# Kernel optimization log

Hardware: AMD Instinct MI355X
Metric: run time of the kernel (lower is better)

The kernel has to match this reference:

```python
import jax, jax.numpy as jnp
import numpy as np

INPUT_SIZE = 512
HIDDEN_SIZE = 512
BATCH = 16384


def setup_inputs() -> dict:
    key = jax.random.key(0)
    ks = jax.random.split(key, 11)
    stdv = 1.0 / np.sqrt(HIDDEN_SIZE)
    in_dim = INPUT_SIZE + HIDDEN_SIZE

    def unif(k, shape):
        return jax.random.uniform(k, shape, jnp.float32, -stdv, stdv)

    inp = {
        "input_": jax.random.normal(ks[0], (BATCH, INPUT_SIZE), jnp.float32),
        "prev_h": jax.random.normal(ks[1], (BATCH, HIDDEN_SIZE), jnp.float32),
        "prev_c": jax.random.normal(ks[2], (BATCH, HIDDEN_SIZE), jnp.float32),
        # gate weights in torch nn.Linear layout: (out=hidden, in=input+hidden)
        "W_i": unif(ks[3], (HIDDEN_SIZE, in_dim)),
        "b_i": unif(ks[4], (HIDDEN_SIZE,)),
        "W_f": unif(ks[5], (HIDDEN_SIZE, in_dim)),
        "b_f": unif(ks[6], (HIDDEN_SIZE,)),
        "W_g": unif(ks[7], (HIDDEN_SIZE, in_dim)),
        "b_g": unif(ks[8], (HIDDEN_SIZE,)),
        "W_o": unif(ks[9], (HIDDEN_SIZE, in_dim)),
        "b_o": unif(ks[10], (HIDDEN_SIZE,)),
    }
    return inp


def reference(input_, prev_h, prev_c, W_i, b_i, W_f, b_f, W_g, b_g, W_o, b_o):
    # x_stack = cat((prev_h, input_), dim=1)  -> (batch, hidden+input)
    x_stack = jnp.concatenate([prev_h, input_], axis=1)
    # Fuse the four gate GEMMs into one: stack weights along out dim.
    W = jnp.concatenate([W_i, W_f, W_o, W_g], axis=0)          # (4H, H+I)
    b = jnp.concatenate([b_i, b_f, b_o, b_g], axis=0)          # (4H,)
    gates = x_stack @ W.T + b                                   # (batch, 4H)
    H = prev_h.shape[1]
    i = jax.nn.sigmoid(gates[:, 0 * H:1 * H])
    f = jax.nn.sigmoid(gates[:, 1 * H:2 * H])
    o = jax.nn.sigmoid(gates[:, 2 * H:3 * H])
    g = jnp.tanh(gates[:, 3 * H:4 * H])
    c = f * prev_c + i * g
    h = jnp.tanh(c) * o
    return (h, c)
```

## Files before the change

### kernel.cpp

```cpp
#include <hip/hip_runtime.h>
#include <hip/hip_bf16.h>
#include <math.h>

typedef unsigned short u16;

#define BATCH 16384
#define HID   512
#define KDIM  1024
#define BM    128
#define BNG   128
#define NSTEP 16

typedef __bf16 bf16x8 __attribute__((ext_vector_type(8)));
typedef float  floatx4 __attribute__((ext_vector_type(4)));

__device__ __forceinline__ void async_copy16(const void* g, void* l) {
  __builtin_amdgcn_global_load_lds(
      (const __attribute__((address_space(1))) void*)g,
      (__attribute__((address_space(3))) void*)l, 16, 0, 0);
}

__device__ __forceinline__ float fast_sigmoid(float x) {
  return 1.0f / (1.0f + __expf(-x));
}
__device__ __forceinline__ float fast_tanh(float x) {
  float e = __expf(-2.0f * fabsf(x));
  float t = (1.0f - e) / (1.0f + e);
  return x >= 0.0f ? t : -t;
}
__device__ __forceinline__ u16 f2bf(float f) {
  return __builtin_bit_cast(u16, __float2bfloat16(f));
}

__global__ __launch_bounds__(256) void pack_kernel(
    const float* __restrict__ input_, const float* __restrict__ prev_h,
    const float* __restrict__ Wi, const float* __restrict__ Wf_,
    const float* __restrict__ Wo, const float* __restrict__ Wg,
    u16* __restrict__ Xb, u16* __restrict__ Wf) {
  int blk = blockIdx.x;
  int k = threadIdx.x * 4;
  if (blk < BATCH) {
    const float* src = (k < HID) ? (prev_h + (size_t)blk * HID + k)
                                 : (input_ + (size_t)blk * HID + (k - HID));
    float4 v = *(const float4*)src;
    ushort4 o;
    o.x = f2bf(v.x); o.y = f2bf(v.y); o.z = f2bf(v.z); o.w = f2bf(v.w);
    *(ushort4*)(Xb + (size_t)blk * KDIM + k) = o;
  } else {
    int grow = blk - BATCH;
    int g = grow >> 9;
    int n = grow & (HID - 1);
    const float* s = g == 0 ? Wi : g == 1 ? Wf_ : g == 2 ? Wo : Wg;
    float4 v = *(const float4*)(s + (size_t)n * KDIM + k);
    ushort4 o;
    o.x = f2bf(v.x); o.y = f2bf(v.y); o.z = f2bf(v.z); o.w = f2bf(v.w);
    size_t d = ((size_t)((g * 32 + (n >> 4)) * 32 + (k >> 5)) * 64 +
                ((k >> 3) & 3) * 16 + (n & 15)) * 8 + (k & 7);
    *(ushort4*)(Wf + d) = o;
  }
}

__global__ __launch_bounds__(512, 2) void lstm_gemm_kernel(
    const u16* __restrict__ Xb, const u16* __restrict__ Wf,
    const float* __restrict__ Bi, const float* __restrict__ Bf,
    const float* __restrict__ Bo, const float* __restrict__ Bg,
    const float* __restrict__ prevC, float* __restrict__ out) {
  __shared__ u16 lds[2][8192];

  const int tid = threadIdx.x;
  const int wave = tid >> 6, lane = tid & 63;
  const int lrow = lane & 15, lquad = lane >> 4;
  const int m_block = blockIdx.x * BM;
  const int ntg = blockIdx.y * 8 + wave;

  const int swz = ((lane & 7) ^ ((lane >> 3) & 7)) * 8;
  const u16* gp[2];
  int lp[2];
#pragma unroll
  for (int i = 0; i < 2; ++i) {
    int li = wave * 2 + i;
    gp[i] = Xb + (size_t)(m_block + li * 8 + (lane >> 3)) * KDIM + swz;
    lp[i] = li * 512;
  }

  floatx4 acc[4][8];
#pragma unroll
  for (int g = 0; g < 4; ++g)
#pragma unroll
    for (int mt = 0; mt < 8; ++mt)
      acc[g][mt] = (floatx4){0.f, 0.f, 0.f, 0.f};

  auto fill = [&](int buf, int S) {
#pragma unroll
    for (int i = 0; i < 2; ++i)
      async_copy16(gp[i] + S * 64, &lds[0][0] + buf * 8192 + lp[i]);
  };

  auto loadB = [&](int S, bf16x8 (&dst)[2][4]) {
#pragma unroll
    for (int kk = 0; kk < 2; ++kk)
#pragma unroll
      for (int g = 0; g < 4; ++g)
        dst[kk][g] = *(const bf16x8*)(
            Wf + (((size_t)(g * 32 + ntg) * 32 + (S * 2 + kk)) << 9) +
            lane * 8);
  };

  auto compute = [&](int buf, bf16x8 (&B)[2][4]) {
    const u16* LA = &lds[buf][0];
#pragma unroll
    for (int kk = 0; kk < 2; ++kk) {
#pragma unroll
      for (int mt = 0; mt < 8; ++mt) {
        bf16x8 a = *(const bf16x8*)
            &LA[(mt * 16 + lrow) * 64 + (((kk * 4 + lquad) ^ (lrow & 7)) * 8)];
#pragma unroll
        for (int g = 0; g < 4; ++g)
          acc[g][mt] = __builtin_amdgcn_mfma_f32_16x16x32_bf16(
              a, B[kk][g], acc[g][mt], 0, 0, 0);
      }
    }
  };

  bf16x8 b0[2][4], b1[2][4];
  loadB(0, b0);
  fill(0, 0);
  for (int S = 0; S < NSTEP; S += 2) {
    __syncthreads();
    fill(1, S + 1);
    loadB(S + 1 < NSTEP ? S + 1 : S, b1);
    compute(0, b0);
    __syncthreads();
    if (S + 2 < NSTEP) {
      fill(0, S + 2);
      loadB(S + 2, b0);
    }
    compute(1, b1);
  }

  const int j = ntg * 16 + lrow;
  const float vbi = Bi[j], vbf = Bf[j], vbo = Bo[j], vbg = Bg[j];
  float* outH = out;
  float* outC = out + (size_t)BATCH * HID;
#pragma unroll
  for (int mt = 0; mt < 8; ++mt) {
    int rowb = m_block + mt * 16 + lquad * 4;
#pragma unroll
    for (int r = 0; r < 4; ++r) {
      int row = rowb + r;
      float gi = fast_sigmoid(acc[0][mt][r] + vbi);
      float gf = fast_sigmoid(acc[1][mt][r] + vbf);
      float go = fast_sigmoid(acc[2][mt][r] + vbo);
      float gg = fast_tanh(acc[3][mt][r] + vbg);
      float c = gf * prevC[row * HID + j] + gi * gg;
      float h = fast_tanh(c) * go;
      outH[row * HID + j] = h;
      outC[row * HID + j] = c;
    }
  }
}

__global__ void lstm_fallback_kernel(
    const float* __restrict__ input_, const float* __restrict__ prev_h,
    const float* __restrict__ prevC,
    const float* __restrict__ Wi, const float* __restrict__ Bi,
    const float* __restrict__ Wf, const float* __restrict__ Bf,
    const float* __restrict__ Wo, const float* __restrict__ Bo,
    const float* __restrict__ Wg, const float* __restrict__ Bg,
    float* __restrict__ out) {
  int idx = blockIdx.x * blockDim.x + threadIdx.x;
  int b = idx / HID, j = idx % HID;
  if (b >= BATCH) return;
  float si = 0.f, sf = 0.f, so = 0.f, sg = 0.f;
  for (int k = 0; k < KDIM; ++k) {
    float x = (k < HID) ? prev_h[b * HID + k] : input_[b * HID + (k - HID)];
    si += x * Wi[j * KDIM + k];
    sf += x * Wf[j * KDIM + k];
    so += x * Wo[j * KDIM + k];
    sg += x * Wg[j * KDIM + k];
  }
  float gi = fast_sigmoid(si + Bi[j]);
  float gf = fast_sigmoid(sf + Bf[j]);
  float go = fast_sigmoid(so + Bo[j]);
  float gg = fast_tanh(sg + Bg[j]);
  float c = gf * prevC[b * HID + j] + gi * gg;
  out[b * HID + j] = fast_tanh(c) * go;
  out[(size_t)BATCH * HID + b * HID + j] = c;
}

extern "C" void kernel_launch(void* const* d_in, const int* in_sizes, int n_in,
                              void* d_out, int out_size, void* d_ws, size_t ws_size,
                              hipStream_t stream) {
  const float* input_ = (const float*)d_in[0];
  const float* prev_h = (const float*)d_in[1];
  const float* prev_c = (const float*)d_in[2];
  const float* W_i = (const float*)d_in[3];
  const float* b_i = (const float*)d_in[4];
  const float* W_f = (const float*)d_in[5];
  const float* b_f = (const float*)d_in[6];
  const float* W_g = (const float*)d_in[7];
  const float* b_g = (const float*)d_in[8];
  const float* W_o = (const float*)d_in[9];
  const float* b_o = (const float*)d_in[10];
  float* out = (float*)d_out;

  const size_t ws_needed =
      (size_t)BATCH * KDIM * sizeof(u16) + (size_t)4 * HID * KDIM * sizeof(u16);

  if (ws_size < ws_needed) {
    int total = BATCH * HID;
    lstm_fallback_kernel<<<(total + 255) / 256, 256, 0, stream>>>(
        input_, prev_h, prev_c, W_i, b_i, W_f, b_f, W_o, b_o, W_g, b_g, out);
    return;
  }

  u16* Xb = (u16*)d_ws;
  u16* Wf = Xb + (size_t)BATCH * KDIM;

  pack_kernel<<<BATCH + 4 * HID, 256, 0, stream>>>(input_, prev_h,
                                                   W_i, W_f, W_o, W_g, Xb, Wf);

  dim3 grid(BATCH / BM, HID / BNG);
  lstm_gemm_kernel<<<grid, 512, 0, stream>>>(Xb, Wf, b_i, b_f, b_o, b_g,
                                             prev_c, out);
}
```

Before: 241.1 us.

## Halve N tile per block, widen K chunk, load B fragments inside compute

The GEMM block drops from 8 waves covering 128 hidden columns to 4 waves covering 64, and the A tile staged in LDS per step doubles to 128 K elements, giving 8 chunks with one barrier each instead of two per pair of steps. B fragments are now loaded straight from global memory inside the compute loop instead of being prefetched into registers a step ahead. The aim is fewer barriers and more blocks in flight. In exchange each A tile is now read by twice as many blocks, and B load latency is exposed without the register prefetch.

After: 243.9 us. No clear change (+1.1%).

```diff
diff --git a/kernel.cpp b/kernel.cpp
--- a/kernel.cpp
+++ b/kernel.cpp
@@ -4,12 +4,13 @@
 
 typedef unsigned short u16;
 
-#define BATCH 16384
-#define HID   512
-#define KDIM  1024
-#define BM    128
-#define BNG   128
-#define NSTEP 16
+#define BATCH  16384
+#define HID    512
+#define KDIM   1024
+#define BM     128
+#define BNG    64
+#define CHUNK  128
+#define NCHUNK 8
 
 typedef __bf16 bf16x8 __attribute__((ext_vector_type(8)));
 typedef float  floatx4 __attribute__((ext_vector_type(4)));
@@ -60,27 +61,28 @@
   }
 }
 
-__global__ __launch_bounds__(512, 2) void lstm_gemm_kernel(
+__global__ __launch_bounds__(256, 2) void lstm_gemm_kernel(
     const u16* __restrict__ Xb, const u16* __restrict__ Wf,
     const float* __restrict__ Bi, const float* __restrict__ Bf,
     const float* __restrict__ Bo, const float* __restrict__ Bg,
     const float* __restrict__ prevC, float* __restrict__ out) {
-  __shared__ u16 lds[2][8192];
+  __shared__ u16 lds[2][16384];
 
   const int tid = threadIdx.x;
   const int wave = tid >> 6, lane = tid & 63;
   const int lrow = lane & 15, lquad = lane >> 4;
   const int m_block = blockIdx.x * BM;
-  const int ntg = blockIdx.y * 8 + wave;
+  const int ntg = blockIdx.y * 4 + wave;
 
   const int swz = ((lane & 7) ^ ((lane >> 3) & 7)) * 8;
-  const u16* gp[2];
-  int lp[2];
-#pragma unroll
-  for (int i = 0; i < 2; ++i) {
-    int li = wave * 2 + i;
-    gp[i] = Xb + (size_t)(m_block + li * 8 + (lane >> 3)) * KDIM + swz;
-    lp[i] = li * 512;
+  const u16* gp[8];
+  int lp[8];
+#pragma unroll
+  for (int i = 0; i < 8; ++i) {
+    int li = wave * 8 + i;
+    int half = li >> 4, j = li & 15;
+    gp[i] = Xb + (size_t)(m_block + j * 8 + (lane >> 3)) * KDIM + half * 64 + swz;
+    lp[i] = half * 8192 + j * 512;
   }
 
   floatx4 acc[4][8];
@@ -90,52 +92,44 @@
     for (int mt = 0; mt < 8; ++mt)
       acc[g][mt] = (floatx4){0.f, 0.f, 0.f, 0.f};
 
-  auto fill = [&](int buf, int S) {
-#pragma unroll
-    for (int i = 0; i < 2; ++i)
-      async_copy16(gp[i] + S * 64, &lds[0][0] + buf * 8192 + lp[i]);
+  auto fill = [&](int buf, int c) {
+#pragma unroll
+    for (int i = 0; i < 8; ++i)
+      async_copy16(gp[i] + c * CHUNK, &lds[0][0] + buf * 16384 + lp[i]);
   };
 
-  auto loadB = [&](int S, bf16x8 (&dst)[2][4]) {
-#pragma unroll
-    for (int kk = 0; kk < 2; ++kk)
-#pragma unroll
-      for (int g = 0; g < 4; ++g)
-        dst[kk][g] = *(const bf16x8*)(
-            Wf + (((size_t)(g * 32 + ntg) * 32 + (S * 2 + kk)) << 9) +
-            lane * 8);
-  };
-
-  auto compute = [&](int buf, bf16x8 (&B)[2][4]) {
-    const u16* LA = &lds[buf][0];
-#pragma unroll
-    for (int kk = 0; kk < 2; ++kk) {
-#pragma unroll
-      for (int mt = 0; mt < 8; ++mt) {
-        bf16x8 a = *(const bf16x8*)
-            &LA[(mt * 16 + lrow) * 64 + (((kk * 4 + lquad) ^ (lrow & 7)) * 8)];
+  auto compute = [&](int buf, int c) {
+#pragma unroll
+    for (int half = 0; half < 2; ++half) {
+      const int t = c * 4 + half * 2;
+      bf16x8 b[2][4];
+#pragma unroll
+      for (int kk = 0; kk < 2; ++kk)
 #pragma unroll
         for (int g = 0; g < 4; ++g)
-          acc[g][mt] = __builtin_amdgcn_mfma_f32_16x16x32_bf16(
-              a, B[kk][g], acc[g][mt], 0, 0, 0);
+          b[kk][g] = *(const bf16x8*)(
+              Wf + (((size_t)(g * 32 + ntg) * 32 + t + kk) << 9) + lane * 8);
+      const u16* LA = &lds[buf][half * 8192];
+#pragma unroll
+      for (int kk = 0; kk < 2; ++kk) {
+#pragma unroll
+        for (int mt = 0; mt < 8; ++mt) {
+          bf16x8 a = *(const bf16x8*)
+              &LA[(mt * 16 + lrow) * 64 + (((kk * 4 + lquad) ^ (lrow & 7)) * 8)];
+#pragma unroll
+          for (int g = 0; g < 4; ++g)
+            acc[g][mt] = __builtin_amdgcn_mfma_f32_16x16x32_bf16(
+                a, b[kk][g], acc[g][mt], 0, 0, 0);
+        }
       }
     }
   };
 
-  bf16x8 b0[2][4], b1[2][4];
-  loadB(0, b0);
   fill(0, 0);
-  for (int S = 0; S < NSTEP; S += 2) {
+  for (int c = 0; c < NCHUNK; ++c) {
     __syncthreads();
-    fill(1, S + 1);
-    loadB(S + 1 < NSTEP ? S + 1 : S, b1);
-    compute(0, b0);
-    __syncthreads();
-    if (S + 2 < NSTEP) {
-      fill(0, S + 2);
-      loadB(S + 2, b0);
-    }
-    compute(1, b1);
+    if (c + 1 < NCHUNK) fill((c + 1) & 1, c + 1);
+    compute(c & 1, c);
   }
 
   const int j = ntg * 16 + lrow;
@@ -215,12 +209,12 @@
   }
 
   u16* Xb = (u16*)d_ws;
-  u16* Wf = Xb + (size_t)BATCH * KDIM;
+  u16* Wfm = Xb + (size_t)BATCH * KDIM;
 
   pack_kernel<<<BATCH + 4 * HID, 256, 0, stream>>>(input_, prev_h,
-                                                   W_i, W_f, W_o, W_g, Xb, Wf);
+                                                   W_i, W_f, W_o, W_g, Xb, Wfm);
 
   dim3 grid(BATCH / BM, HID / BNG);
-  lstm_gemm_kernel<<<grid, 512, 0, stream>>>(Xb, Wf, b_i, b_f, b_o, b_g,
+  lstm_gemm_kernel<<<grid, 256, 0, stream>>>(Xb, Wfm, b_i, b_f, b_o, b_g,
                                              prev_c, out);
 }
```
